# Kernel optimization log

Hardware: AMD Instinct MI355X
Metric: run time of the kernel (lower is better)

The kernel has to match this reference:

```python
import jax, jax.numpy as jnp
import numpy as np

B, T, N = 512, 1024, 48


def setup_inputs() -> dict:
    key = jax.random.key(0)
    k1, k2, k3, k4 = jax.random.split(key, 4)
    potentials = jax.random.normal(k1, (B, T, N), dtype=jnp.float32)
    y_true = jax.random.randint(k2, (B, T), 0, N, dtype=jnp.int32)
    lengths = jax.random.randint(k3, (B,), 1, T + 1, dtype=jnp.int32)
    transitions = jax.random.normal(k4, (N, N), dtype=jnp.float32)
    return {"potentials": potentials, "y_true": y_true,
            "lengths": lengths, "transitions": transitions}


def _crf_log_likelihood(potentials, tags, lengths, trans):
    # potentials: [B,T,N], tags: [B,T] int, lengths: [B] int, trans: [N,N]
    Bv, Tv, Nv = potentials.shape
    t_idx = jnp.arange(Tv)

    # ---- numerator: score of the given tag sequence ----
    unary = jnp.take_along_axis(potentials, tags[..., None], axis=2)[..., 0]  # [B,T]
    unary_mask = (t_idx[None, :] < lengths[:, None]).astype(potentials.dtype)
    unary_score = jnp.sum(unary * unary_mask, axis=1)  # [B]

    trans_scores = trans[tags[:, :-1], tags[:, 1:]]  # [B,T-1]
    pair_mask = (t_idx[None, 1:] < lengths[:, None]).astype(potentials.dtype)
    binary_score = jnp.sum(trans_scores * pair_mask, axis=1)  # [B]
    seq_score = unary_score + binary_score

    # ---- log partition: forward algorithm with length masking ----
    alpha0 = potentials[:, 0, :]  # [B,N]
    pots_rest = jnp.transpose(potentials[:, 1:, :], (1, 0, 2))  # [T-1,B,N]
    valid = (t_idx[1:, None] < lengths[None, :])  # [T-1,B]

    def step(alpha, inp):
        pot_t, v = inp  # [B,N], [B]
        # logsumexp over previous state: alpha[b,i] + trans[i,j]
        new_alpha = jax.nn.logsumexp(alpha[:, :, None] + trans[None, :, :], axis=1) + pot_t
        alpha = jnp.where(v[:, None], new_alpha, alpha)
        return alpha, None

    alpha_final, _ = jax.lax.scan(step, alpha0, (pots_rest, valid))
    log_norm = jax.nn.logsumexp(alpha_final, axis=-1)  # [B]

    return seq_score - log_norm


def reference(potentials, y_true, lengths, transitions):
    ll = _crf_log_likelihood(potentials, y_true.astype(jnp.int32),
                             lengths.astype(jnp.int32), transitions)
    return -ll  # per-sample NLL, shape [B]
```

## Files before the change

### kernel.cpp

```cpp
#include <hip/hip_runtime.h>
#include <cstdint>
#include <cstddef>

constexpr int Bb = 512;
constexpr int Tt = 1024;
constexpr int Nn = 48;
constexpr int SG = 16;
constexpr int NG = Bb / SG;
constexpr int Cc = 16;
constexpr int Lc = Tt / Cc;
constexpr int Wb = 32;

typedef short bf16x8 __attribute__((ext_vector_type(8)));
typedef float f32x4  __attribute__((ext_vector_type(4)));

__device__ __forceinline__ unsigned short bf16_rne(float x) {
    const unsigned int u = __float_as_uint(x);
    return (unsigned short)((u + 0x7FFFu + ((u >> 16) & 1u)) >> 16);
}
__device__ __forceinline__ unsigned short bf16_trunc(float x) {
    return (unsigned short)(__float_as_uint(x) >> 16);
}
__device__ __forceinline__ float safe_log(float x) {
    return __logf(fmaxf(x, 1e-30f));
}

__launch_bounds__(64)
__global__ void crf_fwd_mfma(const float* __restrict__ pot,
                             const int*   __restrict__ lengths,
                             const float* __restrict__ trans,
                             float*       __restrict__ out)
{
    __shared__ float trans_lds[Nn * Nn];
    __shared__ __align__(16) unsigned short ab[SG][64];
    __shared__ __align__(16) float c_buf[16];

    const int lane = threadIdx.x;
    const int ln   = lane & 15;
    const int q    = lane >> 4;
    const int gidx = blockIdx.x >> 4;
    const int c    = blockIdx.x & 15;
    const int s0   = gidx * SG;

    int len4[4];
#pragma unroll
    for (int r = 0; r < 4; ++r) len4[r] = lengths[s0 + q * 4 + r];
    int lmax = lengths[s0 + ln];
#pragma unroll
    for (int off = 8; off > 0; off >>= 1) {
        const int o = __shfl_xor(lmax, off);
        lmax = (o > lmax) ? o : lmax;
    }

    const int start = (c == 0) ? 1 : c * Lc;
    if (c > 0 && start >= lmax) return;
    const int end = ((c + 1) * Lc < lmax) ? (c + 1) * Lc : lmax;

    for (int i = lane; i < Nn * Nn; i += 64) trans_lds[i] = trans[i];
    for (int i = lane; i < SG * 64; i += 64) ((unsigned short*)ab)[i] = 0;
    __syncthreads();

    bf16x8 Bf[3][2];
#pragma unroll
    for (int nt = 0; nt < 3; ++nt)
#pragma unroll
        for (int kc = 0; kc < 2; ++kc)
#pragma unroll
            for (int d = 0; d < 8; ++d) {
                const int i = kc * 32 + q * 8 + d;
                const int j = nt * 16 + ln;
                const float v = (i < Nn) ? __expf(trans_lds[i * Nn + j]) : 0.0f;
                Bf[nt][kc][d] = (short)bf16_rne(v);
            }

    const float* pbase[4];
#pragma unroll
    for (int r = 0; r < 4; ++r)
        pbase[r] = pot + (size_t)(s0 + q * 4 + r) * (Tt * Nn) + ln;

    const int t0 = (c == 0) ? 1 : (start - Wb);

    float pinit[3][4];
#pragma unroll
    for (int nt = 0; nt < 3; ++nt)
#pragma unroll
        for (int r = 0; r < 4; ++r)
            pinit[nt][r] = pbase[r][(size_t)(t0 - 1) * Nn + nt * 16];

    if (ln == 0) {
        f32x4 w = {pinit[0][0], pinit[0][1], pinit[0][2], pinit[0][3]};
        *(f32x4*)(c_buf + 4 * q) = w;
    }
    __syncthreads();
    const f32x4 sh4 = *(const f32x4*)(c_buf + 4 * q);

    float prev[3][4];
    float gacc[4];
#pragma unroll
    for (int r = 0; r < 4; ++r) gacc[r] = (c == 0) ? sh4[r] : 0.0f;
#pragma unroll
    for (int nt = 0; nt < 3; ++nt)
#pragma unroll
        for (int r = 0; r < 4; ++r) {
            const float v = __expf(pinit[nt][r] - sh4[r]);
            prev[nt][r] = v;
            ab[q * 4 + r][nt * 16 + ln] = bf16_trunc(v);
        }
    __syncthreads();

    bf16x8 A0 = *(const bf16x8*)&ab[ln][q * 8];
    bf16x8 A1 = *(const bf16x8*)&ab[ln][32 + q * 8];

    float epv[3][4];
#pragma unroll
    for (int nt = 0; nt < 3; ++nt)
#pragma unroll
        for (int r = 0; r < 4; ++r)
            epv[nt][r] = __expf(pbase[r][(size_t)t0 * Nn + nt * 16]);

    for (int t = t0; t < end; ++t) {
        const bool in_win = (t >= start);
        const int  tn = (t + 1 < Tt) ? (t + 1) : (Tt - 1);
        float pn[3][4];
#pragma unroll
        for (int nt = 0; nt < 3; ++nt)
#pragma unroll
            for (int r = 0; r < 4; ++r)
                pn[nt][r] = pbase[r][(size_t)tn * Nn + nt * 16];

        f32x4 D[3];
#pragma unroll
        for (int nt = 0; nt < 3; ++nt) {
            f32x4 z = {0.0f, 0.0f, 0.0f, 0.0f};
            D[nt] = __builtin_amdgcn_mfma_f32_16x16x32_bf16(A0, Bf[nt][0], z, 0, 0, 0);
            D[nt] = __builtin_amdgcn_mfma_f32_16x16x32_bf16(A1, Bf[nt][1], D[nt], 0, 0, 0);
        }

        float v[3][4];
#pragma unroll
        for (int nt = 0; nt < 3; ++nt)
#pragma unroll
            for (int r = 0; r < 4; ++r)
                v[nt][r] = D[nt][r] * epv[nt][r];

        if (ln == 0) {
            f32x4 w = {v[0][0], v[0][1], v[0][2], v[0][3]};
            *(f32x4*)(c_buf + 4 * q) = w;
        }
        __syncthreads();
        const f32x4 c4 = *(const f32x4*)(c_buf + 4 * q);

        float rr[4];
#pragma unroll
        for (int r = 0; r < 4; ++r) rr[r] = __builtin_amdgcn_rcpf(fmaxf(c4[r], 1e-30f));
#pragma unroll
        for (int r = 0; r < 4; ++r) {
            const float lg = safe_log(c4[r]);
            gacc[r] += (in_win && (t < len4[r])) ? lg : 0.0f;
        }
#pragma unroll
        for (int nt = 0; nt < 3; ++nt)
#pragma unroll
            for (int r = 0; r < 4; ++r) {
                const float ns = (t < len4[r]) ? (v[nt][r] * rr[r]) : prev[nt][r];
                prev[nt][r] = ns;
                ab[q * 4 + r][nt * 16 + ln] = bf16_trunc(ns);
            }
        __syncthreads();

        A0 = *(const bf16x8*)&ab[ln][q * 8];
        A1 = *(const bf16x8*)&ab[ln][32 + q * 8];
#pragma unroll
        for (int nt = 0; nt < 3; ++nt)
#pragma unroll
            for (int r = 0; r < 4; ++r)
                epv[nt][r] = __expf(pn[nt][r]);
    }

    float G[4];
#pragma unroll
    for (int r = 0; r < 4; ++r) {
        float rs = prev[0][r] + prev[1][r] + prev[2][r];
#pragma unroll
        for (int off = 8; off > 0; off >>= 1) rs += __shfl_xor(rs, off);
        const bool active_chunk = (c == 0) || (c * Lc < len4[r]);
        const bool last = active_chunk && (len4[r] <= (c + 1) * Lc);
        const float lgr = safe_log(rs);
        G[r] = gacc[r] + (last ? lgr : 0.0f);
    }
    if (ln == 0) {
#pragma unroll
        for (int r = 0; r < 4; ++r) atomicAdd(&out[s0 + q * 4 + r], G[r]);
    }
}

__launch_bounds__(64)
__global__ void crf_gold(const float* __restrict__ pot,
                         const int*   __restrict__ ytrue,
                         const int*   __restrict__ lengths,
                         const float* __restrict__ trans,
                         float*       __restrict__ out)
{
    __shared__ float trans_lds[Nn * Nn];
    const int b    = blockIdx.x;
    const int lane = threadIdx.x;
    const int len  = lengths[b];

    for (int i = lane; i < Nn * Nn; i += 64) trans_lds[i] = trans[i];
    __syncthreads();

    const int*   yrow = ytrue + (size_t)b * Tt;
    const float* prow = pot + (size_t)b * Tt * Nn;

    float gold = 0.0f;
#pragma unroll
    for (int k = 0; k < Tt / 64; ++k) {
        const int   t    = lane + 64 * k;
        const int   yt   = yrow[t];
        const int   ytm1 = yrow[(t > 0) ? (t - 1) : 0];
        const float u    = prow[(size_t)t * Nn + yt];
        const float tr   = trans_lds[ytm1 * Nn + yt];
        const float m1   = (t < len) ? 1.0f : 0.0f;
        const float m2   = (t >= 1 && t < len) ? 1.0f : 0.0f;
        gold = fmaf(m1, u, gold);
        gold = fmaf(m2, tr, gold);
    }
#pragma unroll
    for (int off = 32; off > 0; off >>= 1) gold += __shfl_xor(gold, off);
    if (lane == 0) atomicAdd(&out[b], -gold);
}

extern "C" void kernel_launch(void* const* d_in, const int* in_sizes, int n_in,
                              void* d_out, int out_size, void* d_ws, size_t ws_size,
                              hipStream_t stream)
{
    const float* pot   = (const float*)d_in[0];
    const int*   ytrue = (const int*)  d_in[1];
    const int*   lens  = (const int*)  d_in[2];
    const float* trans = (const float*)d_in[3];
    float*       out   = (float*)d_out;

    hipMemsetAsync(out, 0, (size_t)out_size * sizeof(float), stream);
    crf_gold<<<dim3(Bb), dim3(64), 0, stream>>>(pot, ytrue, lens, trans, out);
    crf_fwd_mfma<<<dim3(NG * Cc), dim3(64), 0, stream>>>(pot, lens, trans, out);
}
```

Before: 216.7 us.

## Fuse gold-score kernel into forward kernel and replace LDS barriers with shuffles

Merges the gold-path scoring into the forward MFMA kernel, using blockIdx as the sample index since the grid has exactly B blocks, which removes one launch. The per-step scale broadcast through LDS plus __syncthreads is replaced by lane shuffles, and the A-operand exchange relies on a compiler memory fence instead of a barrier, since the block is a single wavefront. The potentials prefetch is deepened to three steps ahead, the LDS row is padded to 72 to reduce bank conflicts, and truncation is switched to round-to-nearest bf16. The risk is that dropping the barriers depends on single-wave execution order, and the extra gold work runs serially before the recurrence in every block.

Result: faster. 209.4 us (-3.4%).

```diff
diff --git a/kernel.cpp b/kernel.cpp
--- a/kernel.cpp
+++ b/kernel.cpp
@@ -10,6 +10,7 @@
 constexpr int Cc = 16;
 constexpr int Lc = Tt / Cc;
 constexpr int Wb = 32;
+constexpr int AP = 72;
 
 typedef short bf16x8 __attribute__((ext_vector_type(8)));
 typedef float f32x4  __attribute__((ext_vector_type(4)));
@@ -18,22 +19,19 @@
     const unsigned int u = __float_as_uint(x);
     return (unsigned short)((u + 0x7FFFu + ((u >> 16) & 1u)) >> 16);
 }
-__device__ __forceinline__ unsigned short bf16_trunc(float x) {
-    return (unsigned short)(__float_as_uint(x) >> 16);
-}
 __device__ __forceinline__ float safe_log(float x) {
     return __logf(fmaxf(x, 1e-30f));
 }
 
 __launch_bounds__(64)
-__global__ void crf_fwd_mfma(const float* __restrict__ pot,
-                             const int*   __restrict__ lengths,
-                             const float* __restrict__ trans,
-                             float*       __restrict__ out)
+__global__ void crf_fused(const float* __restrict__ pot,
+                          const int*   __restrict__ ytrue,
+                          const int*   __restrict__ lengths,
+                          const float* __restrict__ trans,
+                          float*       __restrict__ out)
 {
     __shared__ float trans_lds[Nn * Nn];
-    __shared__ __align__(16) unsigned short ab[SG][64];
-    __shared__ __align__(16) float c_buf[16];
+    __shared__ __align__(16) unsigned short ab[SG][AP];
 
     const int lane = threadIdx.x;
     const int ln   = lane & 15;
@@ -42,6 +40,31 @@
     const int c    = blockIdx.x & 15;
     const int s0   = gidx * SG;
 
+    for (int i = lane; i < Nn * Nn; i += 64) trans_lds[i] = trans[i];
+    for (int i = lane; i < SG * AP; i += 64) ((unsigned short*)ab)[i] = 0;
+    __syncthreads();
+
+    {
+        const int    b    = blockIdx.x;
+        const int    lenb = lengths[b];
+        const int*   yrow = ytrue + (size_t)b * Tt;
+        const float* prow = pot + (size_t)b * Tt * Nn;
+        float gold = 0.0f;
+#pragma unroll
+        for (int k = 0; k < Tt / 64; ++k) {
+            const int   t    = lane + 64 * k;
+            const int   yt   = yrow[t];
+            const int   ytm1 = yrow[(t > 0) ? (t - 1) : 0];
+            const float u    = prow[(size_t)t * Nn + yt];
+            const float tr   = trans_lds[ytm1 * Nn + yt];
+            gold += (t < lenb) ? u : 0.0f;
+            gold += (t >= 1 && t < lenb) ? tr : 0.0f;
+        }
+#pragma unroll
+        for (int off = 32; off > 0; off >>= 1) gold += __shfl_xor(gold, off);
+        if (lane == 0) atomicAdd(&out[b], -gold);
+    }
+
     int len4[4];
 #pragma unroll
     for (int r = 0; r < 4; ++r) len4[r] = lengths[s0 + q * 4 + r];
@@ -55,10 +78,6 @@
     const int start = (c == 0) ? 1 : c * Lc;
     if (c > 0 && start >= lmax) return;
     const int end = ((c + 1) * Lc < lmax) ? (c + 1) * Lc : lmax;
-
-    for (int i = lane; i < Nn * Nn; i += 64) trans_lds[i] = trans[i];
-    for (int i = lane; i < SG * 64; i += 64) ((unsigned short*)ab)[i] = 0;
-    __syncthreads();
 
     bf16x8 Bf[3][2];
 #pragma unroll
@@ -87,12 +106,9 @@
         for (int r = 0; r < 4; ++r)
             pinit[nt][r] = pbase[r][(size_t)(t0 - 1) * Nn + nt * 16];
 
-    if (ln == 0) {
-        f32x4 w = {pinit[0][0], pinit[0][1], pinit[0][2], pinit[0][3]};
-        *(f32x4*)(c_buf + 4 * q) = w;
-    }
-    __syncthreads();
-    const f32x4 sh4 = *(const f32x4*)(c_buf + 4 * q);
+    float sh4[4];
+#pragma unroll
+    for (int r = 0; r < 4; ++r) sh4[r] = __shfl(pinit[0][r], lane & 48);
 
     float prev[3][4];
     float gacc[4];
@@ -104,29 +120,34 @@
         for (int r = 0; r < 4; ++r) {
             const float v = __expf(pinit[nt][r] - sh4[r]);
             prev[nt][r] = v;
-            ab[q * 4 + r][nt * 16 + ln] = bf16_trunc(v);
-        }
-    __syncthreads();
-
+            ab[q * 4 + r][nt * 16 + ln] = bf16_rne(v);
+        }
+    asm volatile("" ::: "memory");
     bf16x8 A0 = *(const bf16x8*)&ab[ln][q * 8];
     bf16x8 A1 = *(const bf16x8*)&ab[ln][32 + q * 8];
-
-    float epv[3][4];
-#pragma unroll
-    for (int nt = 0; nt < 3; ++nt)
-#pragma unroll
-        for (int r = 0; r < 4; ++r)
+    asm volatile("" ::: "memory");
+
+    float epv[3][4], pn1[3][4], pn2[3][4];
+#pragma unroll
+    for (int nt = 0; nt < 3; ++nt)
+#pragma unroll
+        for (int r = 0; r < 4; ++r) {
             epv[nt][r] = __expf(pbase[r][(size_t)t0 * Nn + nt * 16]);
+            const int ta = (t0 + 1 < Tt) ? t0 + 1 : Tt - 1;
+            const int tb = (t0 + 2 < Tt) ? t0 + 2 : Tt - 1;
+            pn1[nt][r] = pbase[r][(size_t)ta * Nn + nt * 16];
+            pn2[nt][r] = pbase[r][(size_t)tb * Nn + nt * 16];
+        }
 
     for (int t = t0; t < end; ++t) {
         const bool in_win = (t >= start);
-        const int  tn = (t + 1 < Tt) ? (t + 1) : (Tt - 1);
-        float pn[3][4];
+        const int  t3 = (t + 3 < Tt) ? (t + 3) : (Tt - 1);
+        float pnew[3][4];
 #pragma unroll
         for (int nt = 0; nt < 3; ++nt)
 #pragma unroll
             for (int r = 0; r < 4; ++r)
-                pn[nt][r] = pbase[r][(size_t)tn * Nn + nt * 16];
+                pnew[nt][r] = pbase[r][(size_t)t3 * Nn + nt * 16];
 
         f32x4 D[3];
 #pragma unroll
@@ -143,12 +164,9 @@
             for (int r = 0; r < 4; ++r)
                 v[nt][r] = D[nt][r] * epv[nt][r];
 
-        if (ln == 0) {
-            f32x4 w = {v[0][0], v[0][1], v[0][2], v[0][3]};
-            *(f32x4*)(c_buf + 4 * q) = w;
-        }
-        __syncthreads();
-        const f32x4 c4 = *(const f32x4*)(c_buf + 4 * q);
+        float c4[4];
+#pragma unroll
+        for (int r = 0; r < 4; ++r) c4[r] = __shfl(v[0][r], lane & 48);
 
         float rr[4];
 #pragma unroll
@@ -164,17 +182,21 @@
             for (int r = 0; r < 4; ++r) {
                 const float ns = (t < len4[r]) ? (v[nt][r] * rr[r]) : prev[nt][r];
                 prev[nt][r] = ns;
-                ab[q * 4 + r][nt * 16 + ln] = bf16_trunc(ns);
+                ab[q * 4 + r][nt * 16 + ln] = bf16_rne(ns);
             }
-        __syncthreads();
-
+        asm volatile("" ::: "memory");
         A0 = *(const bf16x8*)&ab[ln][q * 8];
         A1 = *(const bf16x8*)&ab[ln][32 + q * 8];
-#pragma unroll
-        for (int nt = 0; nt < 3; ++nt)
-#pragma unroll
-            for (int r = 0; r < 4; ++r)
-                epv[nt][r] = __expf(pn[nt][r]);
+        asm volatile("" ::: "memory");
+
+#pragma unroll
+        for (int nt = 0; nt < 3; ++nt)
+#pragma unroll
+            for (int r = 0; r < 4; ++r) {
+                epv[nt][r] = __expf(pn1[nt][r]);
+                pn1[nt][r] = pn2[nt][r];
+                pn2[nt][r] = pnew[nt][r];
+            }
     }
 
     float G[4];
@@ -192,42 +214,6 @@
 #pragma unroll
         for (int r = 0; r < 4; ++r) atomicAdd(&out[s0 + q * 4 + r], G[r]);
     }
-}
-
-__launch_bounds__(64)
-__global__ void crf_gold(const float* __restrict__ pot,
-                         const int*   __restrict__ ytrue,
-                         const int*   __restrict__ lengths,
-                         const float* __restrict__ trans,
-                         float*       __restrict__ out)
-{
-    __shared__ float trans_lds[Nn * Nn];
-    const int b    = blockIdx.x;
-    const int lane = threadIdx.x;
-    const int len  = lengths[b];
-
-    for (int i = lane; i < Nn * Nn; i += 64) trans_lds[i] = trans[i];
-    __syncthreads();
-
-    const int*   yrow = ytrue + (size_t)b * Tt;
-    const float* prow = pot + (size_t)b * Tt * Nn;
-
-    float gold = 0.0f;
-#pragma unroll
-    for (int k = 0; k < Tt / 64; ++k) {
-        const int   t    = lane + 64 * k;
-        const int   yt   = yrow[t];
-        const int   ytm1 = yrow[(t > 0) ? (t - 1) : 0];
-        const float u    = prow[(size_t)t * Nn + yt];
-        const float tr   = trans_lds[ytm1 * Nn + yt];
-        const float m1   = (t < len) ? 1.0f : 0.0f;
-        const float m2   = (t >= 1 && t < len) ? 1.0f : 0.0f;
-        gold = fmaf(m1, u, gold);
-        gold = fmaf(m2, tr, gold);
-    }
-#pragma unroll
-    for (int off = 32; off > 0; off >>= 1) gold += __shfl_xor(gold, off);
-    if (lane == 0) atomicAdd(&out[b], -gold);
 }
 
 extern "C" void kernel_launch(void* const* d_in, const int* in_sizes, int n_in,
@@ -241,6 +227,5 @@
     float*       out   = (float*)d_out;
 
     hipMemsetAsync(out, 0, (size_t)out_size * sizeof(float), stream);
-    crf_gold<<<dim3(Bb), dim3(64), 0, stream>>>(pot, ytrue, lens, trans, out);
-    crf_fwd_mfma<<<dim3(NG * Cc), dim3(64), 0, stream>>>(pot, lens, trans, out);
-}
+    crf_fused<<<dim3(NG * Cc), dim3(64), 0, stream>>>(pot, ytrue, lens, trans, out);
+}
```
